# Performance work log

Measured on AMD Instinct MI355X. Metric: run time of the kernel, lower is better.

Reference implementation:

```python
import jax, jax.numpy as jnp
import numpy as np
from jax import lax

PATCH = 16  # get_patch patch_size; crop taken deterministically at (0,0) (original uses random offsets)
K = 5       # predicted kernel size (kernel_v.view(b,5,5))


def setup_inputs() -> dict:
    key = jax.random.key(0)
    ks = jax.random.split(key, 6)
    B, Cf, H, W = 16, 32, 64, 64
    Ci, Hi, Wi = 3, 512, 512
    return {
        "feature": jax.random.normal(ks[0], (B, Cf, H, W), dtype=jnp.float32),
        "img": jax.random.normal(ks[1], (B, Ci, Hi, Wi), dtype=jnp.float32),
        "conv_w": jax.random.normal(ks[2], (16, 32, 16, 16), dtype=jnp.float32) * 0.02,
        "conv_b": jax.random.normal(ks[3], (16,), dtype=jnp.float32) * 0.02,
        "lin_w": jax.random.normal(ks[4], (25, 144), dtype=jnp.float32) * 0.05,
        "lin_b": jax.random.normal(ks[5], (25,), dtype=jnp.float32) * 0.05,
    }


def reference(feature, img, conv_w, conv_b, lin_w, lin_b):
    B, C, H, W = img.shape
    # --- kernel predictor (eval mode: dropout is identity) ---
    patch = feature[:, :, :PATCH, :PATCH]  # deterministic top-left 16x16 crop
    f = lax.conv_general_dilated(
        patch, conv_w, window_strides=(1, 1), padding=[(1, 1), (1, 1)],
        dimension_numbers=("NCHW", "OIHW", "NCHW"))
    f = f + conv_b[None, :, None, None]            # [B,16,3,3]
    f = f.reshape(B, -1)                           # flatten -> [B,144]
    f = jax.nn.gelu(f, approximate=False)          # torch GELU default = exact erf
    kernel_v = f @ lin_w.T + lin_b                 # [B,25]
    # --- per-sample 5x5 filtering (kornia.filter2D: reflect pad, correlation,
    #     same kernel broadcast over channels) fused as one grouped depthwise conv ---
    k = jnp.broadcast_to(kernel_v.reshape(B, 1, K, K), (B, C, K, K)).reshape(B * C, 1, K, K)
    pad = K // 2
    xp = jnp.pad(img, ((0, 0), (0, 0), (pad, pad), (pad, pad)), mode="reflect")
    xp = xp.reshape(1, B * C, H + 2 * pad, W + 2 * pad)
    out = lax.conv_general_dilated(
        xp, k, window_strides=(1, 1), padding="VALID",
        feature_group_count=B * C,
        dimension_numbers=("NCHW", "OIHW", "NCHW"))
    return out.reshape(B, C, H, W)
```

## Files before the change

kernel.cpp:

```cpp
#include <hip/hip_runtime.h>
#include <math.h>


#define B_  16
#define C_  3
#define H_  512
#define W_  512

__global__ __launch_bounds__(256) void patch_conv_kernel(
    const float* __restrict__ feature,
    const float* __restrict__ conv_w,
    const float* __restrict__ conv_b,
    float* __restrict__ g_out)
{
    __shared__ float patch_raw[17 + 8192 + 17];
    __shared__ float red[9][4];
    float* patch = patch_raw + 17;

    int blk = blockIdx.x;
    int b   = blk >> 4;
    int oc  = blk & 15;
    int tid = threadIdx.x;

    const float* fb = feature + (size_t)b * 32 * 4096;
    const float* wb = conv_w + (size_t)oc * 8192;

    if (tid < 17) { patch_raw[tid] = 0.f; patch_raw[17 + 8192 + tid] = 0.f; }

    for (int i = tid; i < 8192; i += 256) {
        int ic = i >> 8;
        int r  = i & 255;
        patch[i] = fb[ic * 4096 + (r >> 4) * 64 + (r & 15)];
    }

    float wreg[32];
    #pragma unroll
    for (int ic = 0; ic < 32; ic++) wreg[ic] = wb[ic * 256 + tid];

    __syncthreads();

    int kh = tid >> 4;
    int kw = tid & 15;

    float acc[9];
    #pragma unroll
    for (int k = 0; k < 9; k++) acc[k] = 0.f;

    #pragma unroll 4
    for (int ic = 0; ic < 32; ic++) {
        int base = ic * 256 + tid;
        float wv = wreg[ic];
        #pragma unroll
        for (int di = 0; di < 3; di++) {
            #pragma unroll
            for (int dj = 0; dj < 3; dj++) {
                acc[di * 3 + dj] += patch[base + (di - 1) * 16 + (dj - 1)] * wv;
            }
        }
    }

    #pragma unroll
    for (int di = 0; di < 3; di++) {
        #pragma unroll
        for (int dj = 0; dj < 3; dj++) {
            bool ok = ((unsigned)(kh + di - 1) < 16u) &&
                      ((unsigned)(kw + dj - 1) < 16u);
            if (!ok) acc[di * 3 + dj] = 0.f;
        }
    }

    #pragma unroll
    for (int k = 0; k < 9; k++) {
        float v = acc[k];
        #pragma unroll
        for (int off = 32; off > 0; off >>= 1)
            v += __shfl_xor(v, off, 64);
        acc[k] = v;
    }
    int wid  = tid >> 6;
    int lane = tid & 63;
    if (lane == 0) {
        #pragma unroll
        for (int k = 0; k < 9; k++) red[k][wid] = acc[k];
    }
    __syncthreads();
    if (tid < 9) {
        float s = red[tid][0] + red[tid][1] + red[tid][2] + red[tid][3];
        s += conv_b[oc];
        float g = 0.5f * s * (1.0f + erff(s * 0.70710678118654752f));
        g_out[(b * 16 + oc) * 9 + tid] = g;
    }
}

__global__ __launch_bounds__(256) void kv_kernel(
    const float* __restrict__ g_in,
    const float* __restrict__ lin_w,
    const float* __restrict__ lin_b,
    float* __restrict__ kv_out)
{
    __shared__ float wsh[25 * 144];
    __shared__ float gsh[144];
    int b   = blockIdx.x;
    int tid = threadIdx.x;

    for (int i = tid; i < 25 * 144; i += 256) wsh[i] = lin_w[i];
    if (tid < 144) gsh[tid] = g_in[b * 144 + tid];
    __syncthreads();

    if (tid < 25) {
        float acc = lin_b[tid];
        #pragma unroll 8
        for (int j = 0; j < 144; j++) acc += gsh[j] * wsh[tid * 144 + j];
        kv_out[b * 25 + tid] = acc;
    }
}

#define TSX  64
#define TSY  128

__device__ __forceinline__ int reflect_idx(int v, int n) {
    v = (v < 0) ? -v : v;
    v = (v >= n) ? (2 * n - 2 - v) : v;
    return v;
}

template <bool XFAST>
__device__ __forceinline__ void dw_tile(
    const float* __restrict__ ip, float* __restrict__ op,
    const float* w, int ty0, int tx0, int tx, int tyl)
{
    int gx0 = tx0 + tx;
    int xid[8];
    if (!XFAST) {
        #pragma unroll
        for (int j = 0; j < 8; j++) xid[j] = reflect_idx(gx0 - 2 + j, W_);
    }

    float acc[8][4];
    #pragma unroll
    for (int i = 0; i < 8; i++)
        #pragma unroll
        for (int j = 0; j < 4; j++) acc[i][j] = 0.f;

    float win[4][8];

    #pragma unroll
    for (int r = 0; r < 4; r++) {
        int gy = reflect_idx(ty0 + tyl + r - 2, H_);
        const float* rowp = ip + (size_t)gy * W_;
        if (XFAST) {
            const float* rp = rowp + gx0;
            float2 a = *(const float2*)(rp - 2);
            float4 m = *(const float4*)(rp);
            float2 c = *(const float2*)(rp + 4);
            win[r][0] = a.x; win[r][1] = a.y;
            win[r][2] = m.x; win[r][3] = m.y; win[r][4] = m.z; win[r][5] = m.w;
            win[r][6] = c.x; win[r][7] = c.y;
        } else {
            #pragma unroll
            for (int j = 0; j < 8; j++) win[r][j] = rowp[xid[j]];
        }
    }

    #pragma unroll
    for (int r = 0; r < 12; r++) {
        const float* x = win[r & 3];
        #pragma unroll
        for (int orow = 0; orow < 8; orow++) {
            int dy = r - orow;
            if (dy >= 0 && dy < 5) {
                #pragma unroll
                for (int dx = 0; dx < 5; dx++) {
                    float wv = w[dy * 5 + dx];
                    #pragma unroll
                    for (int oc = 0; oc < 4; oc++)
                        acc[orow][oc] += wv * x[oc + dx];
                }
            }
        }
        if (r + 4 < 12) {
            int rn = r + 4;
            int gy = reflect_idx(ty0 + tyl + rn - 2, H_);
            const float* rowp = ip + (size_t)gy * W_;
            float* wdst = win[r & 3];
            if (XFAST) {
                const float* rp = rowp + gx0;
                float2 a = *(const float2*)(rp - 2);
                float4 m = *(const float4*)(rp);
                float2 c = *(const float2*)(rp + 4);
                wdst[0] = a.x; wdst[1] = a.y;
                wdst[2] = m.x; wdst[3] = m.y; wdst[4] = m.z; wdst[5] = m.w;
                wdst[6] = c.x; wdst[7] = c.y;
            } else {
                #pragma unroll
                for (int j = 0; j < 8; j++) wdst[j] = rowp[xid[j]];
            }
        }
    }

    #pragma unroll
    for (int orow = 0; orow < 8; orow++) {
        float4 o;
        o.x = acc[orow][0]; o.y = acc[orow][1];
        o.z = acc[orow][2]; o.w = acc[orow][3];
        *(float4*)&op[(size_t)(ty0 + tyl + orow) * W_ + gx0] = o;
    }
}

__global__ __launch_bounds__(256) void depthwise_kernel(
    const float* __restrict__ img,
    const float* __restrict__ kv,
    float* __restrict__ out)
{
    int bc   = blockIdx.y;
    int b    = bc / C_;
    int tile = blockIdx.x;
    int tyi  = tile >> 3;
    int txi  = tile & 7;
    int ty0  = tyi * TSY;
    int tx0  = txi * TSX;

    int tid = threadIdx.x;
    int tx  = (tid & 15) * 4;
    int tyl = (tid >> 4) * 8;

    float w[25];
    {
        const float* kvp = kv + b * 25;
        #pragma unroll
        for (int i = 0; i < 25; i++)
            w[i] = __int_as_float(
                __builtin_amdgcn_readfirstlane(__float_as_int(kvp[i])));
    }

    const float* ip = img + (size_t)bc * H_ * W_;
    float* op       = out + (size_t)bc * H_ * W_;

    if (txi >= 1 && txi <= 6)
        dw_tile<true >(ip, op, w, ty0, tx0, tx, tyl);
    else
        dw_tile<false>(ip, op, w, ty0, tx0, tx, tyl);
}

extern "C" void kernel_launch(void* const* d_in, const int* in_sizes, int n_in,
                              void* d_out, int out_size, void* d_ws, size_t ws_size,
                              hipStream_t stream) {
    const float* feature = (const float*)d_in[0];
    const float* img     = (const float*)d_in[1];
    const float* conv_w  = (const float*)d_in[2];
    const float* conv_b  = (const float*)d_in[3];
    const float* lin_w   = (const float*)d_in[4];
    const float* lin_b   = (const float*)d_in[5];
    float* out = (float*)d_out;

    float* g_ws  = (float*)d_ws;
    float* kv_ws = g_ws + 2304;

    patch_conv_kernel<<<B_ * 16, 256, 0, stream>>>(feature, conv_w, conv_b, g_ws);
    kv_kernel<<<B_, 256, 0, stream>>>(g_ws, lin_w, lin_b, kv_ws);

    dim3 grid(32, B_ * C_);
    depthwise_kernel<<<grid, 256, 0, stream>>>(img, kv_ws, out);
}
```

Before: 132.7 us.

## Retile depthwise filter to full-width row strips with nontemporal stores

Each depthwise block now covers a full 512-wide strip of 16 rows instead of a 64x128 tile, with 128 threads spanning the width. Only the leftmost and rightmost threads take a branchy reflect path, which replaces the per-block templated slow/fast split. Output writes use nontemporal stores to avoid polluting cache. The grid grows from 32 to 32 blocks per plane with the same count, but row-wise access is more contiguous, while the vertical halo overhead per block increases.

Result: slower. 139.2 us (+4.9%).

```diff
diff --git a/kernel.cpp b/kernel.cpp
--- a/kernel.cpp
+++ b/kernel.cpp
@@ -6,6 +6,8 @@
 #define C_  3
 #define H_  512
 #define W_  512
+
+typedef float nfloat4 __attribute__((ext_vector_type(4)));
 
 __global__ __launch_bounds__(256) void patch_conv_kernel(
     const float* __restrict__ feature,
@@ -115,8 +117,7 @@
     }
 }
 
-#define TSX  64
-#define TSY  128
+#define RPB  16
 
 __device__ __forceinline__ int reflect_idx(int v, int n) {
     v = (v < 0) ? -v : v;
@@ -124,17 +125,35 @@
     return v;
 }
 
-template <bool XFAST>
-__device__ __forceinline__ void dw_tile(
-    const float* __restrict__ ip, float* __restrict__ op,
-    const float* w, int ty0, int tx0, int tx, int tyl)
+__global__ __launch_bounds__(256) void depthwise_kernel(
+    const float* __restrict__ img,
+    const float* __restrict__ kv,
+    float* __restrict__ out)
 {
-    int gx0 = tx0 + tx;
-    int xid[8];
-    if (!XFAST) {
-        #pragma unroll
-        for (int j = 0; j < 8; j++) xid[j] = reflect_idx(gx0 - 2 + j, W_);
-    }
+    int bc  = blockIdx.y;
+    int b   = bc / C_;
+    int yb0 = blockIdx.x * RPB;
+
+    int tid = threadIdx.x;
+    int xid = tid & 127;
+    int tx  = xid * 4;
+    int yg  = tid >> 7;
+    int ty  = yb0 + yg * 8;
+
+    float w[25];
+    {
+        const float* kvp = kv + b * 25;
+        #pragma unroll
+        for (int i = 0; i < 25; i++)
+            w[i] = __int_as_float(
+                __builtin_amdgcn_readfirstlane(__float_as_int(kvp[i])));
+    }
+
+    const float* ip = img + (size_t)bc * H_ * W_;
+    float* op       = out + (size_t)bc * H_ * W_;
+
+    bool edgeL = (tx == 0);
+    bool edgeR = (tx == W_ - 4);
 
     float acc[8][4];
     #pragma unroll
@@ -144,22 +163,25 @@
 
     float win[4][8];
 
+    #define LOADROW(r, dst)                                              \
+    do {                                                                 \
+        int gy = reflect_idx(ty + (r) - 2, H_);                          \
+        const float* rowp = ip + (size_t)gy * W_;                        \
+        const float* rp   = rowp + tx;                                   \
+        float2 a, c;                                                     \
+        if (edgeL) { a.x = rowp[2];  a.y = rowp[1]; }                    \
+        else       { a = *(const float2*)(rp - 2); }                     \
+        float4 m = *(const float4*)rp;                                   \
+        if (edgeR) { c.x = rowp[W_-2]; c.y = rowp[W_-3]; }               \
+        else       { c = *(const float2*)(rp + 4); }                     \
+        (dst)[0] = a.x; (dst)[1] = a.y;                                  \
+        (dst)[2] = m.x; (dst)[3] = m.y; (dst)[4] = m.z; (dst)[5] = m.w;  \
+        (dst)[6] = c.x; (dst)[7] = c.y;                                  \
+    } while (0)
+
     #pragma unroll
     for (int r = 0; r < 4; r++) {
-        int gy = reflect_idx(ty0 + tyl + r - 2, H_);
-        const float* rowp = ip + (size_t)gy * W_;
-        if (XFAST) {
-            const float* rp = rowp + gx0;
-            float2 a = *(const float2*)(rp - 2);
-            float4 m = *(const float4*)(rp);
-            float2 c = *(const float2*)(rp + 4);
-            win[r][0] = a.x; win[r][1] = a.y;
-            win[r][2] = m.x; win[r][3] = m.y; win[r][4] = m.z; win[r][5] = m.w;
-            win[r][6] = c.x; win[r][7] = c.y;
-        } else {
-            #pragma unroll
-            for (int j = 0; j < 8; j++) win[r][j] = rowp[xid[j]];
-        }
+        LOADROW(r, win[r]);
     }
 
     #pragma unroll
@@ -179,67 +201,20 @@
             }
         }
         if (r + 4 < 12) {
-            int rn = r + 4;
-            int gy = reflect_idx(ty0 + tyl + rn - 2, H_);
-            const float* rowp = ip + (size_t)gy * W_;
             float* wdst = win[r & 3];
-            if (XFAST) {
-                const float* rp = rowp + gx0;
-                float2 a = *(const float2*)(rp - 2);
-                float4 m = *(const float4*)(rp);
-                float2 c = *(const float2*)(rp + 4);
-                wdst[0] = a.x; wdst[1] = a.y;
-                wdst[2] = m.x; wdst[3] = m.y; wdst[4] = m.z; wdst[5] = m.w;
-                wdst[6] = c.x; wdst[7] = c.y;
-            } else {
-                #pragma unroll
-                for (int j = 0; j < 8; j++) wdst[j] = rowp[xid[j]];
-            }
-        }
-    }
+            LOADROW(r + 4, wdst);
+        }
+    }
+    #undef LOADROW
 
     #pragma unroll
     for (int orow = 0; orow < 8; orow++) {
-        float4 o;
+        nfloat4 o;
         o.x = acc[orow][0]; o.y = acc[orow][1];
         o.z = acc[orow][2]; o.w = acc[orow][3];
-        *(float4*)&op[(size_t)(ty0 + tyl + orow) * W_ + gx0] = o;
-    }
-}
-
-__global__ __launch_bounds__(256) void depthwise_kernel(
-    const float* __restrict__ img,
-    const float* __restrict__ kv,
-    float* __restrict__ out)
-{
-    int bc   = blockIdx.y;
-    int b    = bc / C_;
-    int tile = blockIdx.x;
-    int tyi  = tile >> 3;
-    int txi  = tile & 7;
-    int ty0  = tyi * TSY;
-    int tx0  = txi * TSX;
-
-    int tid = threadIdx.x;
-    int tx  = (tid & 15) * 4;
-    int tyl = (tid >> 4) * 8;
-
-    float w[25];
-    {
-        const float* kvp = kv + b * 25;
-        #pragma unroll
-        for (int i = 0; i < 25; i++)
-            w[i] = __int_as_float(
-                __builtin_amdgcn_readfirstlane(__float_as_int(kvp[i])));
-    }
-
-    const float* ip = img + (size_t)bc * H_ * W_;
-    float* op       = out + (size_t)bc * H_ * W_;
-
-    if (txi >= 1 && txi <= 6)
-        dw_tile<true >(ip, op, w, ty0, tx0, tx, tyl);
-    else
-        dw_tile<false>(ip, op, w, ty0, tx0, tx, tyl);
+        __builtin_nontemporal_store(
+            o, (nfloat4*)&op[(size_t)(ty + orow) * W_ + tx]);
+    }
 }
 
 extern "C" void kernel_launch(void* const* d_in, const int* in_sizes, int n_in,
@@ -259,6 +234,6 @@
     patch_conv_kernel<<<B_ * 16, 256, 0, stream>>>(feature, conv_w, conv_b, g_ws);
     kv_kernel<<<B_, 256, 0, stream>>>(g_ws, lin_w, lin_b, kv_ws);
 
-    dim3 grid(32, B_ * C_);
+    dim3 grid(H_ / RPB, B_ * C_);
     depthwise_kernel<<<grid, 256, 0, stream>>>(img, kv_ws, out);
 }
```
